# Optimization experiments

Hardware: AMD Instinct MI355X
Metric: run time of the kernel (lower is better)

Reference implementation:

```python
import jax, jax.numpy as jnp
import numpy as np

# Static trigram-LM trie configuration (uniform branching K per node).
V_ = 32000; N_ = 3; K_ = 32; S_ = 32; SOS_ = 0; B_ = 32; L_ = 8
U_ = V_ + 1
N_BI = V_ * K_                    # number of bigram nodes
O_ = U_ + N_BI + 1                # offsets/logbs length (bigram block + sentinel)
N_TRI = N_BI * K_                 # number of trigram leaves
G_ = N_TRI
P_ = O_ + G_                      # logps length


def _build_trie():
    """Valid CSR-style flattened trie: children of node at position q live at
    [offsets[q]+q, offsets[q+1]+q+1); every node has exactly K children with
    sorted token ids 0..K-1. ids[p-U_] is the token id of node at position p."""
    rng = np.random.default_rng(0)
    offsets = np.empty(O_, np.int64)
    # unigram v's children occupy positions [U_+v*K_, U_+(v+1)*K_)
    offsets[:U_] = U_ + np.arange(U_) * (K_ - 1)
    # bigram j (position U_+j) children occupy [O_+j*K_, O_+(j+1)*K_)
    offsets[U_:] = (O_ - U_) + np.arange(N_BI + 1) * (K_ - 1)
    ids = np.empty(P_ - U_, np.int32)
    ids[:N_BI] = np.arange(N_BI) % K_       # bigram node token ids
    ids[N_BI] = 0                           # sentinel slot at position O_-1
    ids[N_BI + 1:] = np.arange(N_TRI) % K_  # trigram leaf token ids
    logps = (-rng.uniform(0.1, 10.0, P_)).astype(np.float32)
    logbs = (-rng.uniform(0.01, 2.0, O_)).astype(np.float32)
    return offsets.astype(np.int32), ids, logps, logbs


def setup_inputs() -> dict:
    key = jax.random.key(0)
    k1, k2 = jax.random.split(key)
    offsets, ids, logps, logbs = _build_trie()
    # tokens in [0, 2K): half of them miss in the trie -> exercises backoff path
    hist = jax.random.randint(k1, (L_, B_), 0, 2 * K_, dtype=jnp.int32)
    hidx = jax.random.randint(k2, (B_,), 0, L_, dtype=jnp.int32)
    return {"hist": hist, "hidx": hidx, "offsets": jnp.asarray(offsets),
            "ids": jnp.asarray(ids), "logps": jnp.asarray(logps),
            "logbs": jnp.asarray(logbs), "sos": SOS_, "V": V_, "N": N_,
            "G": G_, "S": S_}


def reference(hist, hidx, offsets, ids, logps, logbs, sos, V, N, G, S):
    B = hist.shape[1]
    M = B * V
    O = offsets.shape[0]
    P = logps.shape[0]
    shift = 0 if 0 <= sos < V else 1
    U = V + shift + 1 % N
    if N == 1:
        return jnp.broadcast_to(logps[:V], (B, V))
    # Always left-pad N-1 sos tokens (equivalent to torch's rem padding; the
    # subsequent window gather makes extra padding harmless).
    pad = N - 1
    hist = jnp.concatenate([jnp.full((pad, B), sos, hist.dtype), hist])
    hidx = hidx + pad
    # context = the N-1 tokens at positions hidx-(N-1) .. hidx-1, per batch
    pos = hidx[None, :] - (N - 1) + jnp.arange(N - 1)[:, None]   # (N-1, B)
    ctx = jnp.take_along_axis(hist, pos, axis=0)                  # (N-1, B)
    if shift:
        ctx = jnp.where(ctx == sos, V, ctx)
    ctx = ctx.astype(ids.dtype)
    srange = jnp.arange(S)
    # first M entries: candidate words v per batch; last B: context pointer
    desc = jnp.concatenate([jnp.tile(jnp.arange(V, dtype=jnp.int32), B),
                            ctx[-1].astype(jnp.int32)])
    last_logps = jnp.tile(logps[:V], B)                           # (M,)
    last_backoffs = jnp.repeat(logbs[desc[M:]], V)                # (M,)
    found = jnp.ones(M + B, bool)
    for n in range(1, N):
        hist_n = jnp.concatenate([jnp.repeat(ctx[-n], V), ctx[-min(n + 1, N - 1)]])
        desc_starts = offsets[desc] + desc
        desc_ends = offsets[desc + 1] + desc + 1
        pos_desc = desc_starts[:, None] + srange[None, :]         # (M+B, S)
        ext = desc_ends[:, None] > pos_desc
        ids_ = ids[jnp.minimum(pos_desc, P - 1) - U]
        ext = ext & (hist_n[:, None] == ids_)
        found = ext.any(1) & found
        desc = jnp.where(found, jnp.where(ext, pos_desc, 0).sum(1), desc)
        logps_desc = logps[desc[:M]]
        if n == N - 1:
            cur_backoffs = jnp.zeros_like(last_backoffs)
        else:
            cur_backoffs = jnp.repeat(
                jnp.where(found[M:], logbs[jnp.minimum(desc[M:], O - 1)], 0.0), V)
        clobber = jnp.isfinite(logps_desc) & found[:M]
        cur_logps = jnp.where(clobber, logps_desc,
                              last_logps + cur_backoffs + last_backoffs)
        last_backoffs = jnp.where(clobber, cur_backoffs, 0.0)
        last_logps = jnp.where(jnp.repeat(hidx >= n, V), cur_logps, last_logps)
    return last_logps.reshape(B, V)
```

## Files before the change

kernel.cpp:

```cpp
#include <hip/hip_runtime.h>
#include <math.h>


#define MAXN 8
#define BG   16
#define WI   37
#define WO   41

struct PerB {
  int   ctx[MAXN];
  float bo[MAXN];
  float b1;
  int   hp;
};

__device__ __forceinline__ bool find_child(const int* __restrict__ offsets,
                                           const int* __restrict__ ids,
                                           int q, int t, int U, int P, int S,
                                           int* pos_out) {
  int start = offsets[q] + q;
  int end   = offsets[q + 1] + q + 1;
  int n = end - start;
  if (n > S) n = S;
  if (n <= 0) return false;
  int j = (t < n - 1) ? t : (n - 1);
  if (j < 0) j = 0;
  int x = ids[min(start + j, P - 1) - U];
  if (x == t) { *pos_out = start + j; return true; }
  if (x < t) return false;
  int lo = 0, hi = j - 1;
  while (lo < hi) {
    int mid = (lo + hi) >> 1;
    int xm = ids[min(start + mid, P - 1) - U];
    if (xm < t) lo = mid + 1; else hi = mid;
  }
  if (lo < j) {
    int xm = ids[min(start + lo, P - 1) - U];
    if (xm == t) { *pos_out = start + lo; return true; }
  }
  return false;
}

__global__ void lm_prep(const int* __restrict__ hist, const int* __restrict__ hidx,
                        const int* __restrict__ offsets, const int* __restrict__ ids,
                        const float* __restrict__ logbs,
                        const int* __restrict__ sos_p, const int* __restrict__ N_p,
                        const int* __restrict__ S_p,
                        PerB* __restrict__ pb, int V, int B, int L, int O, int P) {
  int b = blockIdx.x * blockDim.x + threadIdx.x;
  if (b >= B) return;
  int sos = *sos_p, N = *N_p, S = *S_p;
  if (N <= 1) return;
  int shift = (0 <= sos && sos < V) ? 0 : 1;
  int U = V + shift + 1 % N;
  int pad = N - 1;
  int hp = hidx[b] + pad;
  PerB o;
  o.hp = hp;
  for (int k = 0; k < N - 1; ++k) {
    int r = hp - (N - 1) + k;
    int tok = (r < pad) ? sos : hist[(r - pad) * B + b];
    if (shift && tok == sos) tok = V;
    o.ctx[k] = tok;
  }
  o.b1 = logbs[o.ctx[N - 2]];
  int desc = o.ctx[N - 2];
  bool found = true;
  for (int n = 1; n <= N - 2; ++n) {
    int t = o.ctx[(N - 1) - min(n + 1, N - 1)];
    if (found) {
      int pos;
      found = find_child(offsets, ids, desc, t, U, P, S, &pos);
      if (found) desc = pos;
    }
    o.bo[n] = found ? logbs[min(desc, O - 1)] : 0.0f;
  }
  pb[b] = o;
}

__device__ __forceinline__ float score_v(const int* __restrict__ offsets,
                                         const int* __restrict__ ids,
                                         const float* __restrict__ logps,
                                         const PerB* __restrict__ pbb,
                                         int v, float lp0,
                                         int N, int U, int O, int P, int S) {
  float last_lp = lp0;
  float last_bo = pbb->b1;
  int hp = pbb->hp;
  int desc = v;
  bool found = true;
  float cur_lp = lp0;
  for (int n = 1; n <= N - 1; ++n) {
    int t = pbb->ctx[(N - 1) - n];
    if (found) {
      int pos;
      found = find_child(offsets, ids, desc, t, U, P, S, &pos);
      if (found) { desc = pos; cur_lp = logps[desc]; }
    }
    float cur_bo = (n == N - 1) ? 0.0f : pbb->bo[n];
    bool clobber = isfinite(cur_lp) && found;
    float newlp = clobber ? cur_lp : (last_lp + cur_bo + last_bo);
    last_bo = clobber ? cur_bo : 0.0f;
    if (hp >= n) last_lp = newlp;
  }
  return last_lp;
}

__global__ void __launch_bounds__(64)
lm_main2(const int* __restrict__ offsets, const int* __restrict__ ids,
         const float* __restrict__ logps,
         const int* __restrict__ sos_p, const int* __restrict__ N_p,
         const int* __restrict__ S_p,
         const PerB* __restrict__ pb, float* __restrict__ out,
         int V, int B, int O, int P) {
  __shared__ int   s_t1[BG], s_t0[BG], s_hp[BG];
  __shared__ float s_bo1[BG], s_b1[BG];
  __shared__ int   ids_w[64 * WI];
  __shared__ int   off_w[64 * WO];

  const int tid = threadIdx.x;
  const int v   = blockIdx.x * 64 + tid;
  const int b0  = blockIdx.y * BG;
  const int N = *N_p, S = *S_p, sos = *sos_p;
  const int Nc = (N > 0) ? N : 1;
  const int shift = (0 <= sos && sos < V) ? 0 : 1;
  const int U = V + shift + 1 % Nc;

  const bool fast = (N == 3) && (S == 32);

  if (!fast) {
    if (v < V) {
      float lp0 = logps[v];
      if (N <= 1) {
        for (int i = 0; i < BG; ++i) {
          int b = b0 + i;
          if (b < B) out[(size_t)b * V + v] = lp0;
        }
      } else {
        for (int i = 0; i < BG; ++i) {
          int b = b0 + i;
          if (b < B)
            out[(size_t)b * V + v] = score_v(offsets, ids, logps, pb + b, v,
                                             lp0, N, U, O, P, S);
        }
      }
    }
    return;
  }

  if (tid < BG) {
    int b = b0 + tid;
    if (b < B) {
      const PerB* q = pb + b;
      s_t1[tid]  = q->ctx[1];
      s_t0[tid]  = q->ctx[0];
      s_bo1[tid] = q->bo[1];
      s_b1[tid]  = q->b1;
      s_hp[tid]  = q->hp;
    }
  }
  __syncthreads();
  if (v >= V) return;

  const int idsN = P - U;
  float lp0 = logps[v];
  int ov  = offsets[v];
  int ov1 = offsets[v + 1];
  int start1 = ov + v;
  int n1 = ov1 + 1 - ov;
  if (n1 > 32) n1 = 32;

  int* myids = ids_w + tid * WI;
  int* myoff = off_w + tid * WO;
  int aidx0 = start1 - U;
  int sh_i = 0, sh_o = 0;
  bool vec_ok = (start1 >= 0) && (aidx0 >= 0) &&
                (((aidx0 & ~3) + 36) <= idsN) &&
                (((start1 & ~3) + 40) <= O);
  if (vec_ok) {
    int ab = aidx0 & ~3;
    sh_i = aidx0 - ab;
    const int4* ip = (const int4*)(ids + ab);
#pragma unroll
    for (int k = 0; k < 9; ++k) {
      int4 t = ip[k];
      myids[4 * k + 0] = t.x; myids[4 * k + 1] = t.y;
      myids[4 * k + 2] = t.z; myids[4 * k + 3] = t.w;
    }
    int ob = start1 & ~3;
    sh_o = start1 - ob;
    const int4* op = (const int4*)(offsets + ob);
#pragma unroll
    for (int k = 0; k < 10; ++k) {
      int4 t = op[k];
      myoff[4 * k + 0] = t.x; myoff[4 * k + 1] = t.y;
      myoff[4 * k + 2] = t.z; myoff[4 * k + 3] = t.w;
    }
  } else {
    for (int j = 0; j < 34; ++j) {
      int ii = min(start1 + j, P - 1) - U;
      ii = max(0, min(ii, idsN - 1));
      myids[j] = ids[ii];
      int oo = max(0, min(start1 + j, O - 1));
      myoff[j] = offsets[oo];
    }
  }

#pragma unroll
  for (int i = 0; i < BG; ++i) {
    int b = b0 + i;
    if (b >= B) continue;
    int   t1 = s_t1[i], t0 = s_t0[i], hp = s_hp[i];
    float bo1 = s_bo1[i], last_bo = s_b1[i];
    float last_lp = lp0;

    bool found = false;
    int j1 = 0;
    if (n1 > 0) {
      int jj = (t1 < n1 - 1) ? t1 : (n1 - 1);
      if (jj < 0) jj = 0;
      int x = myids[sh_i + jj];
      if (x == t1) { found = true; j1 = jj; }
      else if (x > t1) {
        int lo = 0, hi = jj - 1;
        while (lo < hi) {
          int mid = (lo + hi) >> 1;
          if (myids[sh_i + mid] < t1) lo = mid + 1; else hi = mid;
        }
        if (lo < jj && myids[sh_i + lo] == t1) { found = true; j1 = lo; }
      }
    }
    int c1 = start1 + j1;
    float lp1 = found ? logps[min(c1, P - 1)] : lp0;

    {
      bool clob = found && isfinite(lp1);
      float nl = clob ? lp1 : (last_lp + bo1 + last_bo);
      last_bo = clob ? bo1 : 0.0f;
      if (hp >= 1) last_lp = nl;
    }

    if (found) {
      int o1 = myoff[sh_o + j1];
      int o2 = myoff[sh_o + j1 + 1];
      int start2 = o1 + c1;
      int n2 = o2 + 1 - o1;
      if (n2 > 32) n2 = 32;
      bool f2 = false;
      float lp2 = 0.0f;
      if (n2 > 0) {
        int jj = (t0 < n2 - 1) ? t0 : (n2 - 1);
        if (jj < 0) jj = 0;
        int c2 = start2 + jj;
        int cc = min(c2, P - 1);
        int ii = max(0, min(cc - U, idsN - 1));
        int   x2  = ids[ii];
        float sp2 = logps[cc];
        if (x2 == t0) { f2 = true; lp2 = sp2; }
        else if (x2 > t0) {
          int lo = 0, hi = jj - 1;
          while (lo < hi) {
            int mid = (lo + hi) >> 1;
            int im = max(0, min(min(start2 + mid, P - 1) - U, idsN - 1));
            if (ids[im] < t0) lo = mid + 1; else hi = mid;
          }
          if (lo < jj) {
            int il = max(0, min(min(start2 + lo, P - 1) - U, idsN - 1));
            if (ids[il] == t0) { f2 = true; lp2 = logps[min(start2 + lo, P - 1)]; }
          }
        }
      }
      bool clob2 = f2 && isfinite(lp2);
      float nl2 = clob2 ? lp2 : (last_lp + last_bo);
      if (hp >= 2) last_lp = nl2;
    } else {
      float nl2 = last_lp + last_bo;
      if (hp >= 2) last_lp = nl2;
    }

    out[(size_t)b * V + v] = last_lp;
  }
}

extern "C" void kernel_launch(void* const* d_in, const int* in_sizes, int n_in,
                              void* d_out, int out_size, void* d_ws, size_t ws_size,
                              hipStream_t stream) {
  const int*   hist    = (const int*)d_in[0];
  const int*   hidx    = (const int*)d_in[1];
  const int*   offsets = (const int*)d_in[2];
  const int*   ids     = (const int*)d_in[3];
  const float* logps   = (const float*)d_in[4];
  const float* logbs   = (const float*)d_in[5];
  const int*   sos_p   = (const int*)d_in[6];
  const int*   N_p     = (const int*)d_in[8];
  const int*   S_p     = (const int*)d_in[10];

  int B = in_sizes[1];
  int L = in_sizes[0] / B;
  int O = in_sizes[2];
  int P = in_sizes[4];
  int V = out_size / B;
  float* out = (float*)d_out;
  PerB* pb = (PerB*)d_ws;

  lm_prep<<<dim3((B + 63) / 64), dim3(64), 0, stream>>>(
      hist, hidx, offsets, ids, logbs, sos_p, N_p, S_p, pb, V, B, L, O, P);

  dim3 grid((V + 63) / 64, (B + BG - 1) / BG);
  lm_main2<<<grid, dim3(64), 0, stream>>>(
      offsets, ids, logps, sos_p, N_p, S_p, pb, out, V, B, O, P);
}
```

Measured before the change: 278.9 us.

## Batch gather addresses then issue all logps/ids loads before compute

Restructures the per-batch loop into three phases: compute all level-1 and level-2 child addresses, issue every logps and ids gather for the group together, then do the backoff arithmetic. This aims to overlap memory latency across batch entries instead of serializing dependent loads per entry. The group size is halved to limit register pressure from the new per-entry arrays, which adds more blocks or passes. The fallback id and offset loading is also split into separate loops with adjusted lengths.

```diff
diff --git a/kernel.cpp b/kernel.cpp
--- a/kernel.cpp
+++ b/kernel.cpp
@@ -3,7 +3,7 @@
 
 
 #define MAXN 8
-#define BG   16
+#define BG   8
 #define WI   37
 #define WO   41
 
@@ -197,23 +197,27 @@
       myoff[4 * k + 2] = t.z; myoff[4 * k + 3] = t.w;
     }
   } else {
-    for (int j = 0; j < 34; ++j) {
+    for (int j = 0; j < 36; ++j) {
       int ii = min(start1 + j, P - 1) - U;
       ii = max(0, min(ii, idsN - 1));
       myids[j] = ids[ii];
+    }
+    for (int j = 0; j < 40; ++j) {
       int oo = max(0, min(start1 + j, O - 1));
       myoff[j] = offsets[oo];
     }
   }
 
+  const int nb = min(BG, B - b0);
+
+  int j1v[BG];
+  int cc1[BG];
+  int cc2[BG];
+  unsigned f1m = 0, l2m = 0;
 #pragma unroll
   for (int i = 0; i < BG; ++i) {
-    int b = b0 + i;
-    if (b >= B) continue;
-    int   t1 = s_t1[i], t0 = s_t0[i], hp = s_hp[i];
-    float bo1 = s_bo1[i], last_bo = s_b1[i];
-    float last_lp = lp0;
-
+    if (i >= nb) { j1v[i] = 0; cc1[i] = v; cc2[i] = v; continue; }
+    int t1 = s_t1[i];
     bool found = false;
     int j1 = 0;
     if (n1 > 0) {
@@ -231,54 +235,87 @@
       }
     }
     int c1 = start1 + j1;
-    float lp1 = found ? logps[min(c1, P - 1)] : lp0;
-
-    {
-      bool clob = found && isfinite(lp1);
-      float nl = clob ? lp1 : (last_lp + bo1 + last_bo);
-      last_bo = clob ? bo1 : 0.0f;
-      if (hp >= 1) last_lp = nl;
-    }
-
-    if (found) {
-      int o1 = myoff[sh_o + j1];
-      int o2 = myoff[sh_o + j1 + 1];
-      int start2 = o1 + c1;
-      int n2 = o2 + 1 - o1;
-      if (n2 > 32) n2 = 32;
-      bool f2 = false;
-      float lp2 = 0.0f;
-      if (n2 > 0) {
-        int jj = (t0 < n2 - 1) ? t0 : (n2 - 1);
-        if (jj < 0) jj = 0;
-        int c2 = start2 + jj;
-        int cc = min(c2, P - 1);
-        int ii = max(0, min(cc - U, idsN - 1));
-        int   x2  = ids[ii];
-        float sp2 = logps[cc];
-        if (x2 == t0) { f2 = true; lp2 = sp2; }
-        else if (x2 > t0) {
-          int lo = 0, hi = jj - 1;
-          while (lo < hi) {
-            int mid = (lo + hi) >> 1;
-            int im = max(0, min(min(start2 + mid, P - 1) - U, idsN - 1));
-            if (ids[im] < t0) lo = mid + 1; else hi = mid;
-          }
-          if (lo < jj) {
-            int il = max(0, min(min(start2 + lo, P - 1) - U, idsN - 1));
-            if (ids[il] == t0) { f2 = true; lp2 = logps[min(start2 + lo, P - 1)]; }
-          }
+    j1v[i] = j1;
+    int a1 = min(c1, P - 1);
+    cc1[i] = a1;
+    int t0 = s_t0[i];
+    int o1 = myoff[sh_o + j1];
+    int o2 = myoff[sh_o + j1 + 1];
+    int start2 = o1 + c1;
+    int n2 = o2 + 1 - o1;
+    if (n2 > 32) n2 = 32;
+    bool l2ok = found && (n2 > 0);
+    int jj2 = (t0 < n2 - 1) ? t0 : (n2 - 1);
+    if (jj2 < 0) jj2 = 0;
+    int c2 = min(start2 + jj2, P - 1);
+    cc2[i] = l2ok ? c2 : a1;
+    f1m |= (found ? 1u : 0u) << i;
+    l2m |= (l2ok ? 1u : 0u) << i;
+  }
+
+  float lp1v[BG];
+  int   x2v[BG];
+  float sp2v[BG];
+#pragma unroll
+  for (int i = 0; i < BG; ++i) lp1v[i] = logps[cc1[i]];
+#pragma unroll
+  for (int i = 0; i < BG; ++i) {
+    int ii = cc2[i] - U;
+    ii = max(0, min(ii, idsN - 1));
+    x2v[i] = ids[ii];
+  }
+#pragma unroll
+  for (int i = 0; i < BG; ++i) sp2v[i] = logps[cc2[i]];
+
+#pragma unroll
+  for (int i = 0; i < BG; ++i) {
+    if (i >= nb) continue;
+    bool found = (f1m >> i) & 1u;
+    bool l2ok  = (l2m >> i) & 1u;
+    int   hp = s_hp[i];
+    float bo1 = s_bo1[i];
+    float last_bo = s_b1[i];
+    float last_lp = lp0;
+
+    float lp1 = found ? lp1v[i] : lp0;
+    bool clob = found && isfinite(lp1);
+    float nl = clob ? lp1 : (last_lp + bo1 + last_bo);
+    last_bo = clob ? bo1 : 0.0f;
+    if (hp >= 1) last_lp = nl;
+
+    bool f2 = false;
+    float lp2 = 0.0f;
+    if (l2ok) {
+      int t0 = s_t0[i];
+      int x2 = x2v[i];
+      if (x2 == t0) { f2 = true; lp2 = sp2v[i]; }
+      else if (x2 > t0) {
+        int j1 = j1v[i];
+        int c1 = start1 + j1;
+        int o1 = myoff[sh_o + j1];
+        int o2 = myoff[sh_o + j1 + 1];
+        int start2 = o1 + c1;
+        int n2 = o2 + 1 - o1;
+        if (n2 > 32) n2 = 32;
+        int jj2 = (t0 < n2 - 1) ? t0 : (n2 - 1);
+        if (jj2 < 0) jj2 = 0;
+        int lo = 0, hi = jj2 - 1;
+        while (lo < hi) {
+          int mid = (lo + hi) >> 1;
+          int im = max(0, min(min(start2 + mid, P - 1) - U, idsN - 1));
+          if (ids[im] < t0) lo = mid + 1; else hi = mid;
+        }
+        if (lo < jj2) {
+          int il = max(0, min(min(start2 + lo, P - 1) - U, idsN - 1));
+          if (ids[il] == t0) { f2 = true; lp2 = logps[min(start2 + lo, P - 1)]; }
         }
       }
-      bool clob2 = f2 && isfinite(lp2);
-      float nl2 = clob2 ? lp2 : (last_lp + last_bo);
-      if (hp >= 2) last_lp = nl2;
-    } else {
-      float nl2 = last_lp + last_bo;
-      if (hp >= 2) last_lp = nl2;
-    }
-
-    out[(size_t)b * V + v] = last_lp;
+    }
+    bool clob2 = f2 && isfinite(lp2);
+    float nl2 = clob2 ? lp2 : (last_lp + last_bo);
+    if (hp >= 2) last_lp = nl2;
+
+    out[(size_t)(b0 + i) * V + v] = last_lp;
   }
 }
 
```

Measured after the change: 280.9 us. Within noise of the previous version (+0.7%).
